# Kernel tuning notes

Hardware: AMD Instinct MI355X
Metric: run time of the kernel (lower is better)

Reference implementation:

```python
import jax, jax.numpy as jnp
import numpy as np

H = 16  # num heads
EPS = 1e-5


def layer_norm(x, g, b):
    mu = jnp.mean(x, axis=-1, keepdims=True)
    var = jnp.var(x, axis=-1, keepdims=True)
    return (x - mu) * jax.lax.rsqrt(var + EPS) * g + b


def setup_inputs() -> dict:
    key = jax.random.key(0)
    ks = jax.random.split(key, 8)
    B, T, D, TE = 4, 4096, 1024, 1024
    s = 0.02  # weight init scale
    return {
        "x": jax.random.normal(ks[0], (B, T, D), jnp.float32),
        "emb": jax.random.normal(ks[1], (B, 1, TE), jnp.float32),
        "gate_msa": jax.random.normal(ks[2], (B, 1, D), jnp.float32),
        "norm_g": jnp.ones((D,), jnp.float32),
        "norm_b": jnp.zeros((D,), jnp.float32),
        "Wq": jax.random.normal(ks[3], (D, D), jnp.float32) * s,
        "bq": jnp.zeros((D,), jnp.float32),
        "Wk": jax.random.normal(ks[4], (D, D), jnp.float32) * s,
        "bk": jnp.zeros((D,), jnp.float32),
        "Wv": jax.random.normal(ks[5], (D, D), jnp.float32) * s,
        "bv": jnp.zeros((D,), jnp.float32),
        "emb_W": jax.random.normal(ks[6], (TE, 2 * D), jnp.float32) * s,
        "emb_b": jnp.zeros((2 * D,), jnp.float32),
        "sn_g": jnp.ones((D,), jnp.float32),
        "sn_b": jnp.zeros((D,), jnp.float32),
        "out_W": jax.random.normal(ks[7], (D, D), jnp.float32) * s,
        "out_b": jnp.zeros((D,), jnp.float32),
    }


def reference(x, emb, gate_msa, norm_g, norm_b, Wq, bq, Wk, bk, Wv, bv,
              emb_W, emb_b, sn_g, sn_b, out_W, out_b):
    B, T, D = x.shape
    dh = D // H
    xn = layer_norm(x, norm_g, norm_b)
    q = (xn @ Wq + bq).reshape(B, T, H, dh)
    k = (xn @ Wk + bk).reshape(B, T, H, dh)
    v = (xn @ Wv + bv).reshape(B, T, H, dh)
    q = jax.nn.softmax(q, axis=-1)      # feature-dim softmax
    k = jax.nn.softmax(k, axis=1)       # temporal softmax
    ctx = jnp.einsum('bnhd,bnhl->bhdl', k, v)  # [B,H,dh,dh] context
    y = jnp.einsum('bnhd,bhdl->bnhl', q, ctx).reshape(B, T, D)
    # StylizationBlock (dropout=0 eval semantics)
    emb_out = jax.nn.silu(emb) @ emb_W + emb_b        # [B,1,2D]
    scale, shift = jnp.split(emb_out, 2, axis=-1)
    h = layer_norm(y, sn_g, sn_b) * (1.0 + scale) + shift
    h = jax.nn.silu(h) @ out_W + out_b
    return x + gate_msa * h
```

## Files before the change

kernel.cpp:

```cpp
#include <hip/hip_runtime.h>
#include <stdint.h>

typedef unsigned short u16;
typedef float f32x4 __attribute__((ext_vector_type(4)));
typedef __bf16 bf16x8 __attribute__((ext_vector_type(8)));

__device__ __forceinline__ float b2f(u16 u) {
    union { unsigned int i; float f; } w; w.i = ((unsigned int)u) << 16; return w.f;
}
__device__ __forceinline__ u16 f2b(float f) {
    union { float f; unsigned int i; } w; w.f = f;
    unsigned int r = w.i + 0x7fffu + ((w.i >> 16) & 1u);
    return (u16)(r >> 16);
}
__device__ __forceinline__ void gload16(const void* g, void* l) {
    __builtin_amdgcn_global_load_lds(
        (const __attribute__((address_space(1))) unsigned int*)g,
        (__attribute__((address_space(3))) unsigned int*)l, 16, 0, 0);
}

__global__ __launch_bounds__(256) void prep_k(
    const float* __restrict__ Wq, const float* __restrict__ Wk, const float* __restrict__ Wv,
    const float* __restrict__ Wo, const float* __restrict__ bq, const float* __restrict__ bk,
    const float* __restrict__ bv, const float* __restrict__ ob,
    u16* __restrict__ WqkvT, u16* __restrict__ WoT, float* __restrict__ biasAll,
    float* __restrict__ zeroBase)
{
    int bz = blockIdx.x, tid = threadIdx.x;
    if (bz < 4096) {
        int z = bz >> 10, rem = bz & 1023;
        const float* src = (z == 0) ? Wq : (z == 1) ? Wk : (z == 2) ? Wv : Wo;
        u16* dst = (z < 3) ? (WqkvT + (size_t)z * 1024 * 1024) : WoT;
        __shared__ u16 tile[32][33];
        int tx = tid & 31, ty = tid >> 5;
        int n0 = (rem & 31) * 32, k0 = (rem >> 5) * 32;
#pragma unroll
        for (int i = 0; i < 4; i++) tile[ty + 8 * i][tx] = f2b(src[(size_t)(k0 + ty + 8 * i) * 1024 + n0 + tx]);
        __syncthreads();
#pragma unroll
        for (int i = 0; i < 4; i++) dst[(size_t)(n0 + ty + 8 * i) * 1024 + k0 + tx] = tile[tx][ty + 8 * i];
    } else if (bz < 4112) {
        int i = (bz - 4096) * 256 + tid;
        float v;
        if (i < 1024) v = bq[i];
        else if (i < 2048) v = bk[i - 1024];
        else if (i < 3072) v = bv[i - 2048];
        else v = ob[i - 3072];
        biasAll[i] = v;
    } else {
        int e = (bz - 4112) * 256 + tid;
        ((float4*)zeroBase)[e] = make_float4(0.f, 0.f, 0.f, 0.f);
    }
}

__global__ __launch_bounds__(256) void ln_x(
    const float* __restrict__ x, const float* __restrict__ g, const float* __restrict__ bt,
    u16* __restrict__ xn)
{
    int row = blockIdx.x, tid = threadIdx.x;
    const float* xr = x + (size_t)row * 1024;
    float4 u = *(const float4*)(xr + tid * 4);
    float v0 = u.x, v1 = u.y, v2 = u.z, v3 = u.w;
    float s = v0 + v1 + v2 + v3;
    float s2 = v0 * v0 + v1 * v1 + v2 * v2 + v3 * v3;
#pragma unroll
    for (int m = 32; m > 0; m >>= 1) { s += __shfl_xor(s, m, 64); s2 += __shfl_xor(s2, m, 64); }
    __shared__ float red[8];
    int w = tid >> 6, lane = tid & 63;
    if (lane == 0) { red[w] = s; red[4 + w] = s2; }
    __syncthreads();
    s = red[0] + red[1] + red[2] + red[3];
    s2 = red[4] + red[5] + red[6] + red[7];
    float mean = s * (1.f / 1024.f);
    float var = s2 * (1.f / 1024.f) - mean * mean;
    float rstd = rsqrtf(var + 1e-5f);
    int c = tid * 4;
    float4 gg = *(const float4*)(g + c);
    float4 bb = *(const float4*)(bt + c);
    ushort4 o;
    o.x = f2b((v0 - mean) * rstd * gg.x + bb.x);
    o.y = f2b((v1 - mean) * rstd * gg.y + bb.y);
    o.z = f2b((v2 - mean) * rstd * gg.z + bb.z);
    o.w = f2b((v3 - mean) * rstd * gg.w + bb.w);
    *(ushort4*)(xn + (size_t)row * 1024 + c) = o;
}

__global__ __launch_bounds__(512, 2) void gemm256(
    const u16* __restrict__ A, const u16* __restrict__ Bt, const float* __restrict__ bias,
    int mode, u16* __restrict__ Qb, u16* __restrict__ Kb, u16* __restrict__ Vb,
    float* __restrict__ colsum, float* __restrict__ Cf,
    const float* __restrict__ Xf, const float* __restrict__ gate)
{
    const int K = 1024;
    __shared__ __align__(16) u16 L[2][2][256 * 64];
    int tid = threadIdx.x, lane = tid & 63, w = tid >> 6;
    int wm = w >> 2, wn = w & 3;
    int NB = gridDim.x;
    int lid = blockIdx.y * NB + blockIdx.x;
    int xcd = lid & 7;
    int i_ = lid >> 3;
    int rowLocal = i_ & 7;
    int colIdx = i_ >> 3;
    size_t rowbase = (size_t)(xcd * 8 + rowLocal) * 256;
    size_t colbase = (size_t)colIdx * 256;
    const u16* Ab = A + rowbase * K;
    const u16* Bb = Bt + colbase * K;
    f32x4 acc[8][4] = {};
    int quad = lane >> 4, mr = lane & 15, swK = mr & 7;
    int srow = lane >> 3;
    int scol = ((lane & 7) ^ srow) * 8;
    u16* A0 = L[0][0]; u16* B0 = L[0][1]; u16* A1 = L[1][0]; u16* B1 = L[1][1];

#define STAGE(ldsmat, gbase, hf, k0) do { \
    _Pragma("unroll") \
    for (int r_ = 0; r_ < 2; r_++) { \
        int rb_ = (hf) * 128 + r_ * 64 + w * 8; \
        gload16((gbase) + (size_t)(rb_ + srow) * 1024 + (k0) + scol, (ldsmat) + rb_ * 64); \
    } } while (0)

#define LDA(dst, src, mh) do { \
    _Pragma("unroll") \
    for (int i2_ = 0; i2_ < 4; i2_++) \
    _Pragma("unroll") \
    for (int kq_ = 0; kq_ < 2; kq_++) \
        dst[i2_ * 2 + kq_] = *(const bf16x8*)&(src)[(wm * 128 + (mh) * 64 + i2_ * 16 + mr) * 64 + (((kq_ * 4 + quad) ^ swK) * 8)]; \
    } while (0)

#define LDB(dst, src, nh) do { \
    _Pragma("unroll") \
    for (int j_ = 0; j_ < 2; j_++) \
    _Pragma("unroll") \
    for (int kq_ = 0; kq_ < 2; kq_++) \
        dst[j_ * 2 + kq_] = *(const bf16x8*)&(src)[(wn * 64 + (nh) * 32 + j_ * 16 + mr) * 64 + (((kq_ * 4 + quad) ^ swK) * 8)]; \
    } while (0)

#define MM(mh, nh, av, bv) do { \
    __builtin_amdgcn_s_setprio(1); \
    _Pragma("unroll") \
    for (int i2_ = 0; i2_ < 4; i2_++) \
    _Pragma("unroll") \
    for (int j_ = 0; j_ < 2; j_++) \
    _Pragma("unroll") \
    for (int kq_ = 0; kq_ < 2; kq_++) \
        acc[(mh) * 4 + i2_][(nh) * 2 + j_] = __builtin_amdgcn_mfma_f32_16x16x32_bf16( \
            av[i2_ * 2 + kq_], bv[j_ * 2 + kq_], acc[(mh) * 4 + i2_][(nh) * 2 + j_], 0, 0, 0); \
    __builtin_amdgcn_s_setprio(0); } while (0)

#define BAR() asm volatile("s_barrier" ::: "memory")
#define VMW(n) asm volatile("s_waitcnt vmcnt(" #n ")" ::: "memory")

    STAGE(A0, Ab, 0, 0); STAGE(A0, Ab, 1, 0);
    STAGE(B0, Bb, 0, 0); STAGE(B0, Bb, 1, 0);
    STAGE(B1, Bb, 0, 64); STAGE(B1, Bb, 1, 64);
    VMW(4);
    BAR();

    bf16x8 a[8], bn0[4], bn1[4];
    for (int t = 0; t < 8; ++t) {
        int k0 = t * 128;
        bool last = (t == 7);
        LDA(a, A0, 0); LDB(bn0, B0, 0);
        STAGE(A1, Ab, 0, k0 + 64);
        BAR(); MM(0, 0, a, bn0); BAR();
        LDB(bn1, B0, 1);
        STAGE(A1, Ab, 1, k0 + 64);
        BAR(); MM(0, 1, a, bn1); BAR();
        LDA(a, A0, 1);
        if (!last) STAGE(B0, Bb, 0, k0 + 128);
        BAR(); MM(1, 1, a, bn1); BAR();
        if (!last) STAGE(B0, Bb, 1, k0 + 128);
        BAR(); MM(1, 0, a, bn0);
        if (last) { VMW(0); } else { VMW(4); }
        BAR();
        LDA(a, A1, 0); LDB(bn0, B1, 0);
        if (!last) STAGE(A0, Ab, 0, k0 + 128);
        BAR(); MM(0, 0, a, bn0); BAR();
        LDB(bn1, B1, 1);
        if (!last) STAGE(A0, Ab, 1, k0 + 128);
        BAR(); MM(0, 1, a, bn1); BAR();
        LDA(a, A1, 1);
        if (!last) STAGE(B1, Bb, 0, k0 + 192);
        BAR(); MM(1, 1, a, bn1); BAR();
        if (!last) STAGE(B1, Bb, 1, k0 + 192);
        BAR(); MM(1, 0, a, bn0);
        if (!last) VMW(4);
        BAR();
    }
#undef STAGE
#undef LDA
#undef LDB
#undef MM
#undef BAR
#undef VMW

    int colj[4]; float bj[4];
#pragma unroll
    for (int j = 0; j < 4; j++) { colj[j] = (int)colbase + wn * 64 + j * 16 + mr; bj[j] = bias[colj[j]]; }
    int creg = (int)colbase + wn * 64;
    if (mode == 0) {
        if (creg < 1024) {
#pragma unroll
            for (int i = 0; i < 8; i++) {
#pragma unroll
                for (int r = 0; r < 4; r++) {
                    size_t row = rowbase + wm * 128 + i * 16 + quad * 4 + r;
                    float v[4], m = -1e30f, ss = 0.f;
#pragma unroll
                    for (int j = 0; j < 4; j++) { v[j] = acc[i][j][r] + bj[j]; m = fmaxf(m, v[j]); }
#pragma unroll
                    for (int s = 1; s < 16; s <<= 1) m = fmaxf(m, __shfl_xor(m, s, 64));
#pragma unroll
                    for (int j = 0; j < 4; j++) { v[j] = __expf(v[j] - m); ss += v[j]; }
#pragma unroll
                    for (int s = 1; s < 16; s <<= 1) ss += __shfl_xor(ss, s, 64);
                    float inv = 1.f / ss;
#pragma unroll
                    for (int j = 0; j < 4; j++) Qb[row * 1024 + colj[j]] = f2b(v[j] * inv);
                }
            }
        } else if (creg < 2048) {
            int b_ = (int)(rowbase >> 12);
            float csum[4] = {};
#pragma unroll
            for (int j = 0; j < 4; j++) {
#pragma unroll
                for (int i = 0; i < 8; i++) {
#pragma unroll
                    for (int r = 0; r < 4; r++) {
                        size_t row = rowbase + wm * 128 + i * 16 + quad * 4 + r;
                        float e = __expf(acc[i][j][r] + bj[j]);
                        Kb[row * 1024 + (colj[j] - 1024)] = f2b(e);
                        csum[j] += e;
                    }
                }
            }
#pragma unroll
            for (int j = 0; j < 4; j++) {
                csum[j] += __shfl_xor(csum[j], 16, 64);
                csum[j] += __shfl_xor(csum[j], 32, 64);
                if (quad == 0) atomicAdd(&colsum[b_ * 1024 + (colj[j] - 1024)], csum[j]);
            }
        } else {
#pragma unroll
            for (int j = 0; j < 4; j++) {
#pragma unroll
                for (int i = 0; i < 8; i++) {
#pragma unroll
                    for (int r = 0; r < 4; r++) {
                        size_t row = rowbase + wm * 128 + i * 16 + quad * 4 + r;
                        Vb[row * 1024 + (colj[j] - 2048)] = f2b(acc[i][j][r] + bj[j]);
                    }
                }
            }
        }
        return;
    }
    int b_ = (int)(rowbase >> 12);
#pragma unroll
    for (int j = 0; j < 4; j++) {
        float gv = gate[b_ * 1024 + colj[j]];
#pragma unroll
        for (int i = 0; i < 8; i++) {
#pragma unroll
            for (int r = 0; r < 4; r++) {
                size_t row = rowbase + wm * 128 + i * 16 + quad * 4 + r;
                float v = acc[i][j][r] + bj[j];
                Cf[row * 1024 + colj[j]] = Xf[row * 1024 + colj[j]] + gv * v;
            }
        }
    }
}

__global__ __launch_bounds__(256) void ctx_k(
    const u16* __restrict__ kbuf, const u16* __restrict__ vbuf,
    const float* __restrict__ colsum, float* __restrict__ ctx)
{
    int ch = blockIdx.x, h = blockIdx.y, b = blockIdx.z;
    __shared__ __align__(16) float Es[16][64];
    __shared__ __align__(16) float Vs[16][64];
    int tid = threadIdx.x;
    int td = tid >> 4, tl = tid & 15;
    int lr = tid >> 4, lc = (tid & 15) * 4;
    const float* cs = colsum + b * 1024 + h * 64 + lc;
    float4 inv4 = make_float4(1.f / cs[0], 1.f / cs[1], 1.f / cs[2], 1.f / cs[3]);
    float acc[4][4] = {};
    size_t rowbase = (size_t)b * 4096 + ch * 512;
    for (int g = 0; g < 32; ++g) {
        size_t base = (rowbase + g * 16 + lr) * 1024 + h * 64 + lc;
        ushort4 kv = *(const ushort4*)&kbuf[base];
        ushort4 vv = *(const ushort4*)&vbuf[base];
        *(float4*)&Es[lr][lc] = make_float4(b2f(kv.x) * inv4.x, b2f(kv.y) * inv4.y,
                                            b2f(kv.z) * inv4.z, b2f(kv.w) * inv4.w);
        *(float4*)&Vs[lr][lc] = make_float4(b2f(vv.x), b2f(vv.y), b2f(vv.z), b2f(vv.w));
        __syncthreads();
#pragma unroll
        for (int n = 0; n < 16; n++) {
            f32x4 e4 = *(const f32x4*)&Es[n][td * 4];
            f32x4 v4 = *(const f32x4*)&Vs[n][tl * 4];
#pragma unroll
            for (int i = 0; i < 4; i++)
#pragma unroll
                for (int j = 0; j < 4; j++) acc[i][j] += e4[i] * v4[j];
        }
        __syncthreads();
    }
    float* cb = ctx + (size_t)(b * 16 + h) * 4096;
#pragma unroll
    for (int i = 0; i < 4; i++)
#pragma unroll
        for (int j = 0; j < 4; j++)
            atomicAdd(&cb[(td * 4 + i) * 64 + tl * 4 + j], acc[i][j]);
}

__global__ __launch_bounds__(256) void embout_k(
    const float* __restrict__ emb, const float* __restrict__ embW, float* __restrict__ eo)
{
    int cb = blockIdx.x, kc = blockIdx.y;
    __shared__ float semb[128];
    int tid = threadIdx.x;
    if (tid < 128) {
        int b = tid >> 5, kk = tid & 31;
        float xv = emb[b * 1024 + kc * 32 + kk];
        semb[tid] = xv / (1.f + __expf(-xv));
    }
    __syncthreads();
    int o = cb * 256 + tid;
    float a0 = 0, a1 = 0, a2 = 0, a3 = 0;
    for (int kk = 0; kk < 32; kk++) {
        float wv = embW[(size_t)(kc * 32 + kk) * 2048 + o];
        a0 += semb[kk] * wv; a1 += semb[32 + kk] * wv;
        a2 += semb[64 + kk] * wv; a3 += semb[96 + kk] * wv;
    }
    atomicAdd(&eo[o], a0);
    atomicAdd(&eo[2048 + o], a1);
    atomicAdd(&eo[4096 + o], a2);
    atomicAdd(&eo[6144 + o], a3);
}

__global__ __launch_bounds__(256) void y_k(
    const u16* __restrict__ q, const float* __restrict__ ctx, u16* __restrict__ y)
{
    int mc = blockIdx.x, h = blockIdx.y, b = blockIdx.z;
    __shared__ __align__(16) u16 Qs[128 * 64];
    __shared__ __align__(16) u16 Cs[64 * 72];
    int tid = threadIdx.x, lane = tid & 63, w = tid >> 6;
    size_t row0 = (size_t)b * 4096 + (size_t)mc * 128;
    const u16* Qb = q + row0 * 1024 + h * 64;
    int sr = tid >> 3, g_ = tid & 7;
    int scb = (g_ ^ (sr & 7)) * 8;
#pragma unroll
    for (int p = 0; p < 4; p++) {
        int r = p * 32 + sr;
        *(uint4*)&Qs[r * 64 + scb] = *(const uint4*)&Qb[(size_t)r * 1024 + g_ * 8];
    }
    const float* Cb = ctx + (size_t)(b * 16 + h) * 4096;
#pragma unroll
    for (int rep = 0; rep < 16; ++rep) {
        int e = tid + rep * 256;
        int d = e >> 6, l = e & 63;
        Cs[l * 72 + d] = f2b(Cb[e]);
    }
    __syncthreads();
    int quad = lane >> 4, mr = lane & 15;
    int swA = mr & 7;
    f32x4 acc[2][4] = {};
#pragma unroll
    for (int kk = 0; kk < 64; kk += 32) {
        bf16x8 a[2], bb[4];
#pragma unroll
        for (int i = 0; i < 2; i++)
            a[i] = *(const bf16x8*)&Qs[(w * 32 + i * 16 + mr) * 64 + ((((kk >> 3) + quad) ^ swA) * 8)];
#pragma unroll
        for (int j = 0; j < 4; j++) bb[j] = *(const bf16x8*)&Cs[(j * 16 + mr) * 72 + kk + quad * 8];
#pragma unroll
        for (int i = 0; i < 2; i++)
#pragma unroll
            for (int j = 0; j < 4; j++)
                acc[i][j] = __builtin_amdgcn_mfma_f32_16x16x32_bf16(a[i], bb[j], acc[i][j], 0, 0, 0);
    }
#pragma unroll
    for (int i = 0; i < 2; i++)
#pragma unroll
        for (int j = 0; j < 4; j++)
#pragma unroll
            for (int r = 0; r < 4; r++) {
                size_t row = row0 + w * 32 + i * 16 + quad * 4 + r;
                int col = h * 64 + j * 16 + mr;
                y[row * 1024 + col] = f2b(acc[i][j][r]);
            }
}

__global__ __launch_bounds__(256) void style_k(
    u16* __restrict__ y, const float* __restrict__ eo, const float* __restrict__ embb,
    const float* __restrict__ sng, const float* __restrict__ snb)
{
    int row = blockIdx.x, tid = threadIdx.x, b = row >> 12;
    u16* yr = y + (size_t)row * 1024;
    ushort4 u = *(const ushort4*)(yr + tid * 4);
    float vv[4] = { b2f(u.x), b2f(u.y), b2f(u.z), b2f(u.w) };
    float s = vv[0] + vv[1] + vv[2] + vv[3];
    float s2 = vv[0] * vv[0] + vv[1] * vv[1] + vv[2] * vv[2] + vv[3] * vv[3];
#pragma unroll
    for (int m = 32; m > 0; m >>= 1) { s += __shfl_xor(s, m, 64); s2 += __shfl_xor(s2, m, 64); }
    __shared__ float red[8];
    int w = tid >> 6, lane = tid & 63;
    if (lane == 0) { red[w] = s; red[4 + w] = s2; }
    __syncthreads();
    s = red[0] + red[1] + red[2] + red[3];
    s2 = red[4] + red[5] + red[6] + red[7];
    float mean = s * (1.f / 1024.f);
    float var = s2 * (1.f / 1024.f) - mean * mean;
    float rstd = rsqrtf(var + 1e-5f);
    int c = tid * 4;
    ushort4 o;
    u16* op = (u16*)&o;
#pragma unroll
    for (int i = 0; i < 4; i++) {
        int cc = c + i;
        float scale = eo[b * 2048 + cc] + embb[cc];
        float shift = eo[b * 2048 + 1024 + cc] + embb[1024 + cc];
        float hn = (vv[i] - mean) * rstd * sng[cc] + snb[cc];
        float hh = hn * (1.f + scale) + shift;
        op[i] = f2b(hh / (1.f + __expf(-hh)));
    }
    *(ushort4*)(yr + c) = o;
}

extern "C" void kernel_launch(void* const* d_in, const int* in_sizes, int n_in,
                              void* d_out, int out_size, void* d_ws, size_t ws_size,
                              hipStream_t stream)
{
    const float* x    = (const float*)d_in[0];
    const float* emb  = (const float*)d_in[1];
    const float* gate = (const float*)d_in[2];
    const float* ng   = (const float*)d_in[3];
    const float* nb   = (const float*)d_in[4];
    const float* Wq   = (const float*)d_in[5];
    const float* bq   = (const float*)d_in[6];
    const float* Wk   = (const float*)d_in[7];
    const float* bk   = (const float*)d_in[8];
    const float* Wv   = (const float*)d_in[9];
    const float* bv   = (const float*)d_in[10];
    const float* embW = (const float*)d_in[11];
    const float* embB = (const float*)d_in[12];
    const float* sng  = (const float*)d_in[13];
    const float* snb  = (const float*)d_in[14];
    const float* Wo   = (const float*)d_in[15];
    const float* ob   = (const float*)d_in[16];
    float* out = (float*)d_out;

    uint8_t* ws = (uint8_t*)d_ws;
    size_t off = 0;
    auto alloc = [&](size_t bytes) { void* p = ws + off; off += (bytes + 255) & ~(size_t)255; return p; };
    u16*   WqkvT   = (u16*)alloc(3072ull * 1024 * 2);
    u16*   WoT     = (u16*)alloc(1024ull * 1024 * 2);
    float* biasAll = (float*)alloc(4096 * 4);
    float* colsum  = (float*)alloc(4096 * 4);
    float* ctx     = (float*)alloc(64ull * 64 * 64 * 4);
    float* embout  = (float*)alloc(4ull * 2048 * 4);
    u16*   XN      = (u16*)alloc(16384ull * 1024 * 2);
    u16*   BUF0    = (u16*)alloc(16384ull * 1024 * 2);
    u16*   BUF1    = (u16*)alloc(16384ull * 1024 * 2);
    u16*   BUF2    = (u16*)alloc(16384ull * 1024 * 2);

    prep_k<<<4380, 256, 0, stream>>>(Wq, Wk, Wv, Wo, bq, bk, bv, ob, WqkvT, WoT, biasAll, colsum);
    ln_x<<<16384, 256, 0, stream>>>(x, ng, nb, XN);
    gemm256<<<dim3(12, 64), 512, 0, stream>>>(XN, WqkvT, biasAll, 0,
                                              BUF0, BUF1, BUF2, colsum, nullptr, nullptr, nullptr);
    ctx_k<<<dim3(8, 16, 4), 256, 0, stream>>>(BUF1, BUF2, colsum, ctx);
    embout_k<<<dim3(8, 32), 256, 0, stream>>>(emb, embW, embout);
    y_k<<<dim3(32, 16, 4), 256, 0, stream>>>(BUF0, ctx, XN);
    style_k<<<16384, 256, 0, stream>>>(XN, embout, embB, sng, snb);
    gemm256<<<dim3(4, 64), 512, 0, stream>>>(XN, WoT, biasAll + 3072, 2,
                                             nullptr, nullptr, nullptr, nullptr, out, x, gate);
}
```

Measured before the change: 453.6 us.

## Load B operand directly from global to registers with 4-deep A LDS ring

Restructures the GEMM main loop so the weight (B) operand is read straight from global memory into registers, one k-step ahead, instead of being staged through LDS. The A operand now uses a four-buffer LDS ring of 64-wide k-slices, prefetched two to three steps ahead with finer-grained waitcnt and barrier placement. Epilogue loops are reordered so the column index is innermost. This frees LDS bandwidth and capacity and cuts shared-memory traffic for B, but relies on uncoalesced 16-byte global loads and more registers held live, which may hurt occupancy.

```diff
diff --git a/kernel.cpp b/kernel.cpp
--- a/kernel.cpp
+++ b/kernel.cpp
@@ -92,7 +92,7 @@
     const float* __restrict__ Xf, const float* __restrict__ gate)
 {
     const int K = 1024;
-    __shared__ __align__(16) u16 L[2][2][256 * 64];
+    __shared__ __align__(16) u16 As[4][256 * 64];
     int tid = threadIdx.x, lane = tid & 63, w = tid >> 6;
     int wm = w >> 2, wn = w & 3;
     int NB = gridDim.x;
@@ -104,37 +104,31 @@
     size_t rowbase = (size_t)(xcd * 8 + rowLocal) * 256;
     size_t colbase = (size_t)colIdx * 256;
     const u16* Ab = A + rowbase * K;
-    const u16* Bb = Bt + colbase * K;
     f32x4 acc[8][4] = {};
     int quad = lane >> 4, mr = lane & 15, swK = mr & 7;
     int srow = lane >> 3;
     int scol = ((lane & 7) ^ srow) * 8;
-    u16* A0 = L[0][0]; u16* B0 = L[0][1]; u16* A1 = L[1][0]; u16* B1 = L[1][1];
-
-#define STAGE(ldsmat, gbase, hf, k0) do { \
-    _Pragma("unroll") \
-    for (int r_ = 0; r_ < 2; r_++) { \
-        int rb_ = (hf) * 128 + r_ * 64 + w * 8; \
-        gload16((gbase) + (size_t)(rb_ + srow) * 1024 + (k0) + scol, (ldsmat) + rb_ * 64); \
-    } } while (0)
-
-#define LDA(dst, src, mh) do { \
+    const u16* Bw = Bt + (size_t)(colbase + wn * 64 + mr) * K + quad * 8;
+
+    bf16x8 aM0[8], aM1[8], bnA0[4], bnA1[4], bnB0[4], bnB1[4];
+
+#define STG(sbuf, k0s, step) do { \
+    int rb_ = (step) * 64 + w * 8; \
+    gload16(Ab + (size_t)(rb_ + srow) * 1024 + (k0s) + scol, (u16*)(sbuf) + rb_ * 64); \
+    } while (0)
+
+#define BL(dst, k0, h, j, kq) \
+    dst = *(const bf16x8*)(Bw + (size_t)((h) * 32 + (j) * 16) * 1024 + (k0) + (kq) * 32)
+
+#define LDA8(dst, bufp, mh) do { \
     _Pragma("unroll") \
     for (int i2_ = 0; i2_ < 4; i2_++) \
     _Pragma("unroll") \
     for (int kq_ = 0; kq_ < 2; kq_++) \
-        dst[i2_ * 2 + kq_] = *(const bf16x8*)&(src)[(wm * 128 + (mh) * 64 + i2_ * 16 + mr) * 64 + (((kq_ * 4 + quad) ^ swK) * 8)]; \
+        dst[i2_ * 2 + kq_] = *(const bf16x8*)&((const u16*)(bufp))[(wm * 128 + (mh) * 64 + i2_ * 16 + mr) * 64 + (((kq_ * 4 + quad) ^ swK) * 8)]; \
     } while (0)
 
-#define LDB(dst, src, nh) do { \
-    _Pragma("unroll") \
-    for (int j_ = 0; j_ < 2; j_++) \
-    _Pragma("unroll") \
-    for (int kq_ = 0; kq_ < 2; kq_++) \
-        dst[j_ * 2 + kq_] = *(const bf16x8*)&(src)[(wn * 64 + (nh) * 32 + j_ * 16 + mr) * 64 + (((kq_ * 4 + quad) ^ swK) * 8)]; \
-    } while (0)
-
-#define MM(mh, nh, av, bv) do { \
+#define MM16(mh, nh, av, bv) do { \
     __builtin_amdgcn_s_setprio(1); \
     _Pragma("unroll") \
     for (int i2_ = 0; i2_ < 4; i2_++) \
@@ -149,47 +143,58 @@
 #define BAR() asm volatile("s_barrier" ::: "memory")
 #define VMW(n) asm volatile("s_waitcnt vmcnt(" #n ")" ::: "memory")
 
-    STAGE(A0, Ab, 0, 0); STAGE(A0, Ab, 1, 0);
-    STAGE(B0, Bb, 0, 0); STAGE(B0, Bb, 1, 0);
-    STAGE(B1, Bb, 0, 64); STAGE(B1, Bb, 1, 64);
-    VMW(4);
+#pragma unroll
+    for (int s_ = 0; s_ < 4; ++s_) STG(As[0], 0, s_);
+#pragma unroll
+    for (int s_ = 0; s_ < 4; ++s_) STG(As[1], 64, s_);
+    STG(As[2], 128, 0);
+    BL(bnA0[0], 0, 0, 0, 0); BL(bnA0[1], 0, 0, 0, 1);
+    BL(bnA0[2], 0, 0, 1, 0); BL(bnA0[3], 0, 0, 1, 1);
+    BL(bnA1[0], 0, 1, 0, 0); BL(bnA1[1], 0, 1, 0, 1);
+    BL(bnA1[2], 0, 1, 1, 0); BL(bnA1[3], 0, 1, 1, 1);
+    VMW(13);
     BAR();
-
-    bf16x8 a[8], bn0[4], bn1[4];
-    for (int t = 0; t < 8; ++t) {
-        int k0 = t * 128;
-        bool last = (t == 7);
-        LDA(a, A0, 0); LDB(bn0, B0, 0);
-        STAGE(A1, Ab, 0, k0 + 64);
-        BAR(); MM(0, 0, a, bn0); BAR();
-        LDB(bn1, B0, 1);
-        STAGE(A1, Ab, 1, k0 + 64);
-        BAR(); MM(0, 1, a, bn1); BAR();
-        LDA(a, A0, 1);
-        if (!last) STAGE(B0, Bb, 0, k0 + 128);
-        BAR(); MM(1, 1, a, bn1); BAR();
-        if (!last) STAGE(B0, Bb, 1, k0 + 128);
-        BAR(); MM(1, 0, a, bn0);
-        if (last) { VMW(0); } else { VMW(4); }
-        BAR();
-        LDA(a, A1, 0); LDB(bn0, B1, 0);
-        if (!last) STAGE(A0, Ab, 0, k0 + 128);
-        BAR(); MM(0, 0, a, bn0); BAR();
-        LDB(bn1, B1, 1);
-        if (!last) STAGE(A0, Ab, 1, k0 + 128);
-        BAR(); MM(0, 1, a, bn1); BAR();
-        LDA(a, A1, 1);
-        if (!last) STAGE(B1, Bb, 0, k0 + 192);
-        BAR(); MM(1, 1, a, bn1); BAR();
-        if (!last) STAGE(B1, Bb, 1, k0 + 192);
-        BAR(); MM(1, 0, a, bn0);
-        if (!last) VMW(4);
-        BAR();
-    }
-#undef STAGE
-#undef LDA
-#undef LDB
-#undef MM
+    LDA8(aM0, As[0], 0);
+
+#define TILE(T, C0, C1, N0, N1) do { \
+    const u16* bufC_ = As[(T) & 3]; \
+    const int kN_ = ((T) + 1) * 64; \
+     \
+    if ((T) < 15) { BL(N0[0], kN_, 0, 0, 0); BL(N0[1], kN_, 0, 0, 1); } \
+    if ((T) + 2 < 16) STG(As[((T) + 2) & 3], ((T) + 2) * 64, 1); \
+    MM16(0, 0, aM0, C0); \
+    BAR(); \
+     \
+    if ((T) < 15) { BL(N0[2], kN_, 0, 1, 0); BL(N0[3], kN_, 0, 1, 1); } \
+    if ((T) + 2 < 16) STG(As[((T) + 2) & 3], ((T) + 2) * 64, 2); \
+    LDA8(aM1, bufC_, 1); \
+    MM16(0, 1, aM0, C1); \
+    BAR(); \
+     \
+    if ((T) < 15) { BL(N1[0], kN_, 1, 0, 0); BL(N1[1], kN_, 1, 0, 1); } \
+    if ((T) + 2 < 16) STG(As[((T) + 2) & 3], ((T) + 2) * 64, 3); \
+    MM16(1, 1, aM1, C1); \
+    if ((T) < 14) { VMW(12); } else if ((T) == 14) { VMW(8); } \
+    BAR(); \
+     \
+    if ((T) < 15) { BL(N1[2], kN_, 1, 1, 0); BL(N1[3], kN_, 1, 1, 1); } \
+    if ((T) + 3 < 16) STG(As[((T) + 3) & 3], ((T) + 3) * 64, 0); \
+    if ((T) < 15) LDA8(aM0, As[((T) + 1) & 3], 0); \
+    MM16(1, 0, aM1, C0); \
+    BAR(); \
+    } while (0)
+
+#pragma unroll 1
+    for (int t2 = 0; t2 < 8; ++t2) {
+        int T = 2 * t2;
+        TILE(T, bnA0, bnA1, bnB0, bnB1);
+        TILE((T + 1), bnB0, bnB1, bnA0, bnA1);
+    }
+#undef TILE
+#undef STG
+#undef BL
+#undef LDA8
+#undef MM16
 #undef BAR
 #undef VMW
 
@@ -222,12 +227,12 @@
             int b_ = (int)(rowbase >> 12);
             float csum[4] = {};
 #pragma unroll
-            for (int j = 0; j < 4; j++) {
-#pragma unroll
-                for (int i = 0; i < 8; i++) {
-#pragma unroll
-                    for (int r = 0; r < 4; r++) {
-                        size_t row = rowbase + wm * 128 + i * 16 + quad * 4 + r;
+            for (int i = 0; i < 8; i++) {
+#pragma unroll
+                for (int r = 0; r < 4; r++) {
+                    size_t row = rowbase + wm * 128 + i * 16 + quad * 4 + r;
+#pragma unroll
+                    for (int j = 0; j < 4; j++) {
                         float e = __expf(acc[i][j][r] + bj[j]);
                         Kb[row * 1024 + (colj[j] - 1024)] = f2b(e);
                         csum[j] += e;
@@ -242,30 +247,31 @@
             }
         } else {
 #pragma unroll
-            for (int j = 0; j < 4; j++) {
-#pragma unroll
-                for (int i = 0; i < 8; i++) {
-#pragma unroll
-                    for (int r = 0; r < 4; r++) {
-                        size_t row = rowbase + wm * 128 + i * 16 + quad * 4 + r;
+            for (int i = 0; i < 8; i++) {
+#pragma unroll
+                for (int r = 0; r < 4; r++) {
+                    size_t row = rowbase + wm * 128 + i * 16 + quad * 4 + r;
+#pragma unroll
+                    for (int j = 0; j < 4; j++)
                         Vb[row * 1024 + (colj[j] - 2048)] = f2b(acc[i][j][r] + bj[j]);
-                    }
                 }
             }
         }
         return;
     }
     int b_ = (int)(rowbase >> 12);
-#pragma unroll
-    for (int j = 0; j < 4; j++) {
-        float gv = gate[b_ * 1024 + colj[j]];
-#pragma unroll
-        for (int i = 0; i < 8; i++) {
-#pragma unroll
-            for (int r = 0; r < 4; r++) {
-                size_t row = rowbase + wm * 128 + i * 16 + quad * 4 + r;
+    float gv[4];
+#pragma unroll
+    for (int j = 0; j < 4; j++) gv[j] = gate[b_ * 1024 + colj[j]];
+#pragma unroll
+    for (int i = 0; i < 8; i++) {
+#pragma unroll
+        for (int r = 0; r < 4; r++) {
+            size_t row = rowbase + wm * 128 + i * 16 + quad * 4 + r;
+#pragma unroll
+            for (int j = 0; j < 4; j++) {
                 float v = acc[i][j][r] + bj[j];
-                Cf[row * 1024 + colj[j]] = Xf[row * 1024 + colj[j]] + gv * v;
+                Cf[row * 1024 + colj[j]] = Xf[row * 1024 + colj[j]] + gv[j] * v;
             }
         }
     }
```

Measured after the change: 669.6 us. 47.6% more time.
